# Performance work log

Hardware: AMD Instinct MI355X
Metric: run time of the kernel (lower is better)

The kernel has to match this reference:

```python
import jax, jax.numpy as jnp
import numpy as np

ALPHA = 0.2  # LeakyReLU negative slope
NEG_INF = -9e15


def setup_inputs() -> dict:
    key = jax.random.key(0)
    k1, k2, k3, k4 = jax.random.split(key, 4)
    N, IN_F, OUT_F = 8192, 512, 256
    h = jax.random.normal(k1, (N, IN_F), dtype=jnp.float32)
    adj = jax.random.randint(k2, (N, N), 0, 2).astype(jnp.float32)
    # xavier_uniform for torch Linear weights
    limW = float(np.sqrt(6.0 / (IN_F + OUT_F)))
    W = jax.random.uniform(k3, (OUT_F, IN_F), dtype=jnp.float32, minval=-limW, maxval=limW)
    lima = float(np.sqrt(6.0 / (2 * OUT_F + 1)))
    a_vec = jax.random.uniform(k4, (2 * OUT_F,), dtype=jnp.float32, minval=-lima, maxval=lima)
    return {"h": h, "adj": adj, "W": W, "a_vec": a_vec}


def reference(h, adj, W, a_vec):
    # Wh = W(h), torch Linear: h @ W.T  -> [N, out]
    Wh = h @ W.T
    F_out = W.shape[0]
    # e_ij = leakyrelu(a . [Wh_i, Wh_j]) = leakyrelu(a1.Wh_i + a2.Wh_j)
    s_src = Wh @ a_vec[:F_out]   # [N] contribution of row i
    s_dst = Wh @ a_vec[F_out:]   # [N] contribution of col j
    e = jax.nn.leaky_relu(s_src[:, None] + s_dst[None, :], negative_slope=ALPHA)  # [N, N]
    scores = jnp.where(adj > 0, e, jnp.float32(NEG_INF))
    attention = jax.nn.softmax(scores, axis=1)
    # dropout is identity in eval mode
    h_prime = attention @ Wh  # [N, out]
    return h_prime, attention
```

## Files before the change

### kernel.cpp

```cpp
#include <hip/hip_runtime.h>
#include <stdint.h>

#define N_NODES 8192
#define IN_F    512
#define OUT_F   256
#define ALPHA   0.2f

typedef __attribute__((ext_vector_type(8))) short bf16x8;
typedef __attribute__((ext_vector_type(4))) float f32x4;

__device__ __forceinline__ uint32_t f32_to_bf16(float f) {
    union { float f; uint32_t u; } v; v.f = f;
    uint32_t u = v.u;
    return (u + 0x7fffu + ((u >> 16) & 1u)) >> 16;
}

__global__ __launch_bounds__(256) void k0_wvec(
    const float* __restrict__ W, const float* __restrict__ a_vec,
    float* __restrict__ w12)
{
    const int t  = threadIdx.x;
    const int nb = blockIdx.x * 8;
    float a1lo = 0.f, a1hi = 0.f, a2lo = 0.f, a2hi = 0.f;
    #pragma unroll
    for (int q = 0; q < 8; q++) {
        int n = nb + q;
        float lo = W[(size_t)n * IN_F + t];
        float hi = W[(size_t)n * IN_F + t + 256];
        float a1 = a_vec[n], a2 = a_vec[OUT_F + n];
        a1lo = fmaf(lo, a1, a1lo); a1hi = fmaf(hi, a1, a1hi);
        a2lo = fmaf(lo, a2, a2lo); a2hi = fmaf(hi, a2, a2hi);
    }
    atomicAdd(&w12[t], a1lo);       atomicAdd(&w12[t + 256], a1hi);
    atomicAdd(&w12[512 + t], a2lo); atomicAdd(&w12[512 + t + 256], a2hi);
}

__global__ __launch_bounds__(256) void ks_svec(
    const float* __restrict__ h, const float* __restrict__ w12,
    float* __restrict__ s_src, float* __restrict__ s_dst)
{
    __shared__ float sw[1024];
    const int t = threadIdx.x;
    #pragma unroll
    for (int q = 0; q < 4; q++) sw[q * 256 + t] = w12[q * 256 + t];
    __syncthreads();
    const int w = t >> 6, ln = t & 63;
    const int i = blockIdx.x * 4 + w;
    const float* hr = h + (size_t)i * IN_F + ln * 8;
    float4 h0 = *(const float4*)hr;
    float4 h1 = *(const float4*)(hr + 4);
    const float* w1 = sw + ln * 8;
    const float* w2 = sw + 512 + ln * 8;
    float v1 = h0.x*w1[0] + h0.y*w1[1] + h0.z*w1[2] + h0.w*w1[3]
             + h1.x*w1[4] + h1.y*w1[5] + h1.z*w1[6] + h1.w*w1[7];
    float v2 = h0.x*w2[0] + h0.y*w2[1] + h0.z*w2[2] + h0.w*w2[3]
             + h1.x*w2[4] + h1.y*w2[5] + h1.z*w2[6] + h1.w*w2[7];
    #pragma unroll
    for (int off = 32; off >= 1; off >>= 1) {
        v1 += __shfl_xor(v1, off, 64);
        v2 += __shfl_xor(v2, off, 64);
    }
    if (ln == 0) { s_src[i] = v1; s_dst[i] = v2; }
}

__global__ __launch_bounds__(256) void k1_wh_pack(
    const float* __restrict__ h, const float* __restrict__ W,
    uint16_t* __restrict__ whf)
{
    const int n0 = blockIdx.x * 64, i0 = blockIdx.y * 64;
    const int t  = threadIdx.x;
    const int tn = t & 15, tm = t >> 4;

    __shared__ float As[32][68];
    __shared__ float Bs[32][68];

    float acc[4][4];
    #pragma unroll
    for (int i = 0; i < 4; i++)
        #pragma unroll
        for (int j = 0; j < 4; j++) acc[i][j] = 0.f;

    for (int k0 = 0; k0 < IN_F; k0 += 32) {
        __syncthreads();
        #pragma unroll
        for (int q = 0; q < 2; q++) {
            int u   = q * 256 + t;
            int row = u >> 3;
            int kf  = (u & 7) * 4;
            float4 va = *(const float4*)&h[(size_t)(i0 + row) * IN_F + k0 + kf];
            As[kf + 0][row] = va.x; As[kf + 1][row] = va.y;
            As[kf + 2][row] = va.z; As[kf + 3][row] = va.w;
            float4 vb = *(const float4*)&W[(size_t)(n0 + row) * IN_F + k0 + kf];
            Bs[kf + 0][row] = vb.x; Bs[kf + 1][row] = vb.y;
            Bs[kf + 2][row] = vb.z; Bs[kf + 3][row] = vb.w;
        }
        __syncthreads();
        #pragma unroll
        for (int kk = 0; kk < 32; kk++) {
            float a[4], b[4];
            *(float4*)a = *(const float4*)&As[kk][tm * 4];
            *(float4*)b = *(const float4*)&Bs[kk][tn * 4];
            #pragma unroll
            for (int i = 0; i < 4; i++)
                #pragma unroll
                for (int j = 0; j < 4; j++) acc[i][j] = fmaf(a[i], b[j], acc[i][j]);
        }
    }

    #pragma unroll
    for (int ii = 0; ii < 4; ii++) {
        int gr = i0 + tm * 4 + ii;
        int ck = gr >> 5;
        int lr = (gr >> 3) & 3;
        int jj = gr & 7;
        #pragma unroll
        for (int jn = 0; jn < 4; jn++) {
            int gc   = n0 + tn * 4 + jn;
            int c    = ck * 16 + (gc >> 4);
            int lane = (gc & 15) + lr * 16;
            whf[(size_t)c * 512 + lane * 8 + jj] = (uint16_t)f32_to_bf16(acc[ii][jn]);
        }
    }
}

__global__ __launch_bounds__(256) void k2_mask_l(
    const float* __restrict__ adj, const float* __restrict__ s_src,
    const float* __restrict__ s_dst, uint64_t* __restrict__ mask,
    float* __restrict__ l_out)
{
    const int i = blockIdx.x;
    const int t = threadIdx.x, w = t >> 6, ln = t & 63;
    const float si = s_src[i];
    const float4* rowv = (const float4*)(adj + (size_t)i * N_NODES);
    const float4* sdv  = (const float4*)s_dst;
    float acc = 0.f;
    #pragma unroll 2
    for (int it = 0; it < 8; it++) {
        int jb = it * 4 + w;
        int v4 = jb * 64 + ln;
        float4 a  = rowv[v4];
        float4 sd = sdv[v4];
        uint64_t b0 = __ballot(a.x > 0.f);
        uint64_t b1 = __ballot(a.y > 0.f);
        uint64_t b2 = __ballot(a.z > 0.f);
        uint64_t b3 = __ballot(a.w > 0.f);
        if (ln == 0) {
            uint64_t* mw = mask + (size_t)i * 128 + jb * 4;
            mw[0] = b0; mw[1] = b1; mw[2] = b2; mw[3] = b3;
        }
        float x, e;
        x = si + sd.x; e = fmaxf(x, ALPHA * x); if (a.x > 0.f) acc += __expf(e);
        x = si + sd.y; e = fmaxf(x, ALPHA * x); if (a.y > 0.f) acc += __expf(e);
        x = si + sd.z; e = fmaxf(x, ALPHA * x); if (a.z > 0.f) acc += __expf(e);
        x = si + sd.w; e = fmaxf(x, ALPHA * x); if (a.w > 0.f) acc += __expf(e);
    }
    #pragma unroll
    for (int off = 32; off >= 1; off >>= 1) acc += __shfl_xor(acc, off, 64);
    __shared__ float red[4];
    if (ln == 0) red[w] = acc;
    __syncthreads();
    if (t == 0) l_out[i] = (red[0] + red[1]) + (red[2] + red[3]);
}

__global__ __launch_bounds__(256, 4) void k3_att_gemm(
    const uint64_t* __restrict__ mask, const float* __restrict__ s_src,
    const float* __restrict__ s_dst, const float* __restrict__ l_in,
    const uint16_t* __restrict__ whf, float* __restrict__ att_out,
    float* __restrict__ partial)
{
    const int rb = blockIdx.x, jc = blockIdx.y;
    const int i0 = rb * 32, jbase = jc * 2048;
    const int t = threadIdx.x, w = t >> 6, ln = t & 63;
    const int mh = w & 1, kh = w >> 1;

    const int m   = mh * 16 + (ln & 15);
    const int kof = (ln >> 4) * 8;
    const int gi  = i0 + m;

    const float sim = s_src[gi];
    const float il  = 1.0f / l_in[gi];

    f32x4 acc[16];
    #pragma unroll
    for (int b = 0; b < 16; b++) acc[b] = (f32x4){0.f, 0.f, 0.f, 0.f};

    const uint64_t* mrow = mask + (size_t)gi * 128 + (jbase >> 8) * 4;
    uint64_t mwv[4];

    for (int it = 0; it < 32; it++) {
        const int j0 = jbase + it * 64;

        if ((it & 3) == 0) {
            const uint64_t* mp = mrow + (it >> 2) * 4;
            mwv[0] = mp[0]; mwv[1] = mp[1]; mwv[2] = mp[2]; mwv[3] = mp[3];
        }

        const float* sp = s_dst + j0 + kh * 32 + kof;
        float4 sd0 = *(const float4*)sp;
        float4 sd1 = *(const float4*)(sp + 4);
        float sdv[8] = {sd0.x, sd0.y, sd0.z, sd0.w, sd1.x, sd1.y, sd1.z, sd1.w};

        const int bbase = ((it & 3) << 4) + (kh << 3) + (kof >> 2);
        float p[8];
        #pragma unroll
        for (int jj = 0; jj < 8; jj++) {
            float x  = sim + sdv[jj];
            float e  = fmaxf(x, ALPHA * x);
            float pe = __expf(e) * il;
            int bidx = bbase + (jj >> 2);
            p[jj] = ((mwv[jj & 3] >> bidx) & 1ull) ? pe : 0.f;
        }

        float* go = att_out + (size_t)gi * N_NODES + j0 + kh * 32 + kof;
        __builtin_nontemporal_store(*(f32x4*)&p[0], (f32x4*)go);
        __builtin_nontemporal_store(*(f32x4*)&p[4], (f32x4*)(go + 4));

        union { bf16x8 v; uint32_t u[4]; } pk;
        #pragma unroll
        for (int q = 0; q < 4; q++)
            pk.u[q] = f32_to_bf16(p[2 * q]) | (f32_to_bf16(p[2 * q + 1]) << 16);
        bf16x8 af = pk.v;

        const uint16_t* src = whf + (((size_t)(j0 >> 5) + kh) << 13) + ln * 8;
        #pragma unroll
        for (int nl = 0; nl < 16; nl++) {
            bf16x8 bfr = *(const bf16x8*)(src + nl * 512);
            acc[nl] = __builtin_amdgcn_mfma_f32_16x16x32_bf16(af, bfr, acc[nl], 0, 0, 0);
        }
    }

    __shared__ float red[2][16][257];
    const int lr = (ln >> 4) * 4;
    if (kh == 1) {
        #pragma unroll
        for (int nl = 0; nl < 16; nl++)
            #pragma unroll
            for (int r = 0; r < 4; r++)
                red[mh][lr + r][nl * 16 + (ln & 15)] = acc[nl][r];
    }
    __syncthreads();
    if (kh == 0) {
        float* pbase = partial + (size_t)jc * ((size_t)N_NODES * OUT_F);
        const int gr0 = i0 + mh * 16 + lr;
        #pragma unroll
        for (int nl = 0; nl < 16; nl++) {
            int gc = nl * 16 + (ln & 15);
            #pragma unroll
            for (int r = 0; r < 4; r++)
                pbase[(size_t)(gr0 + r) * OUT_F + gc] = acc[nl][r] + red[mh][lr + r][gc];
        }
    }
}

__global__ __launch_bounds__(256) void k4_reduce(
    const float* __restrict__ partial, float* __restrict__ hp)
{
    const size_t S = (size_t)N_NODES * OUT_F;
    int idx = (blockIdx.x * 256 + threadIdx.x) * 4;
    float4 a = *(const float4*)(partial + idx);
    float4 b = *(const float4*)(partial + S + idx);
    float4 c = *(const float4*)(partial + 2 * S + idx);
    float4 d = *(const float4*)(partial + 3 * S + idx);
    float4 o;
    o.x = (a.x + b.x) + (c.x + d.x);
    o.y = (a.y + b.y) + (c.y + d.y);
    o.z = (a.z + b.z) + (c.z + d.z);
    o.w = (a.w + b.w) + (c.w + d.w);
    *(float4*)(hp + idx) = o;
}

extern "C" void kernel_launch(void* const* d_in, const int* in_sizes, int n_in,
                              void* d_out, int out_size, void* d_ws, size_t ws_size,
                              hipStream_t stream) {
    (void)in_sizes; (void)n_in; (void)out_size; (void)ws_size;
    const float* h     = (const float*)d_in[0];
    const float* adj   = (const float*)d_in[1];
    const float* W     = (const float*)d_in[2];
    const float* a_vec = (const float*)d_in[3];

    char* ws = (char*)d_ws;
    uint16_t* whf  = (uint16_t*)(ws);
    uint64_t* mask = (uint64_t*)(ws + ((size_t)4 << 20));
    float* partial = (float*)(ws + ((size_t)12 << 20));
    float* w12     = (float*)(ws + ((size_t)44 << 20));
    float* s_src   = (float*)(ws + ((size_t)44 << 20) + 16384);
    float* s_dst   = (float*)(ws + ((size_t)44 << 20) + 16384 + 32768);
    float* l_buf   = (float*)(ws + ((size_t)44 << 20) + 16384 + 65536);

    float* hp  = (float*)d_out;
    float* att = hp + (size_t)N_NODES * OUT_F;

    hipMemsetAsync(w12, 0, 4096, stream);
    k0_wvec<<<32, 256, 0, stream>>>(W, a_vec, w12);
    ks_svec<<<2048, 256, 0, stream>>>(h, w12, s_src, s_dst);
    k1_wh_pack<<<dim3(4, 128), 256, 0, stream>>>(h, W, whf);
    k2_mask_l<<<8192, 256, 0, stream>>>(adj, s_src, s_dst, mask, l_buf);
    k3_att_gemm<<<dim3(256, 4), 256, 0, stream>>>(mask, s_src, s_dst, l_buf, whf, att, partial);
    k4_reduce<<<2048, 256, 0, stream>>>(partial, hp);
}
```

Before: 727.4 us.

## Double-buffer Wh B-tiles into LDS via async global-to-LDS copies

The attention GEMM kernel now stages each 64-row slice of bf16 Wh into a double-buffered LDS tile with global_load_lds, prefetching the next slice while MFMAs consume the current one, rather than having each wave load B fragments straight from global memory. The 64KB buffer is reused for the final reduction scratch, and launch bounds drop to 2 blocks per SU to fit the LDS. The aim is to share B loads across the two M-half waves and hide global latency. The cost is a block-wide barrier and full vmcnt drain every iteration, plus lower occupancy. The mask/row-sum kernel loop is also fully unrolled.

New measurement: 682.5 us. 6.2% less time.

```diff
diff --git a/kernel.cpp b/kernel.cpp
--- a/kernel.cpp
+++ b/kernel.cpp
@@ -13,6 +13,12 @@
     union { float f; uint32_t u; } v; v.f = f;
     uint32_t u = v.u;
     return (u + 0x7fffu + ((u >> 16) & 1u)) >> 16;
+}
+
+__device__ __forceinline__ void async_copy16(const void* g, void* l) {
+    __builtin_amdgcn_global_load_lds(
+        (const __attribute__((address_space(1))) uint32_t*)g,
+        (__attribute__((address_space(3))) uint32_t*)l, 16, 0, 0);
 }
 
 __global__ __launch_bounds__(256) void k0_wvec(
@@ -134,7 +140,7 @@
     const float4* rowv = (const float4*)(adj + (size_t)i * N_NODES);
     const float4* sdv  = (const float4*)s_dst;
     float acc = 0.f;
-    #pragma unroll 2
+    #pragma unroll
     for (int it = 0; it < 8; it++) {
         int jb = it * 4 + w;
         int v4 = jb * 64 + ln;
@@ -162,7 +168,7 @@
     if (t == 0) l_out[i] = (red[0] + red[1]) + (red[2] + red[3]);
 }
 
-__global__ __launch_bounds__(256, 4) void k3_att_gemm(
+__global__ __launch_bounds__(256, 2) void k3_att_gemm(
     const uint64_t* __restrict__ mask, const float* __restrict__ s_src,
     const float* __restrict__ s_dst, const float* __restrict__ l_in,
     const uint16_t* __restrict__ whf, float* __restrict__ att_out,
@@ -173,6 +179,8 @@
     const int t = threadIdx.x, w = t >> 6, ln = t & 63;
     const int mh = w & 1, kh = w >> 1;
 
+    __shared__ uint16_t whf_lds[2][16384];
+
     const int m   = mh * 16 + (ln & 15);
     const int kof = (ln >> 4) * 8;
     const int gi  = i0 + m;
@@ -187,8 +195,30 @@
     const uint64_t* mrow = mask + (size_t)gi * 128 + (jbase >> 8) * 4;
     uint64_t mwv[4];
 
+    {
+        const uint16_t* src = whf + ((size_t)(jbase >> 5)) * 8192;
+        #pragma unroll
+        for (int q = 0; q < 8; q++) {
+            int c = w * 8 + q;
+            async_copy16(src + (size_t)c * 512 + ln * 8, &whf_lds[0][c * 512]);
+        }
+        asm volatile("s_waitcnt vmcnt(0)" ::: "memory");
+        __builtin_amdgcn_s_barrier();
+    }
+
     for (int it = 0; it < 32; it++) {
-        const int j0 = jbase + it * 64;
+        const int j0  = jbase + it * 64;
+        const int cur = it & 1;
+
+        if (it < 31) {
+            const uint16_t* src = whf + ((size_t)((j0 + 64) >> 5)) * 8192;
+            #pragma unroll
+            for (int q = 0; q < 8; q++) {
+                int c = w * 8 + q;
+                async_copy16(src + (size_t)c * 512 + ln * 8,
+                             &whf_lds[cur ^ 1][c * 512]);
+            }
+        }
 
         if ((it & 3) == 0) {
             const uint64_t* mp = mrow + (it >> 2) * 4;
@@ -221,15 +251,19 @@
             pk.u[q] = f32_to_bf16(p[2 * q]) | (f32_to_bf16(p[2 * q + 1]) << 16);
         bf16x8 af = pk.v;
 
-        const uint16_t* src = whf + (((size_t)(j0 >> 5) + kh) << 13) + ln * 8;
+        const uint16_t* bl = &whf_lds[cur][kh * 8192 + ln * 8];
         #pragma unroll
         for (int nl = 0; nl < 16; nl++) {
-            bf16x8 bfr = *(const bf16x8*)(src + nl * 512);
+            bf16x8 bfr = *(const bf16x8*)(bl + nl * 512);
             acc[nl] = __builtin_amdgcn_mfma_f32_16x16x32_bf16(af, bfr, acc[nl], 0, 0, 0);
         }
-    }
-
-    __shared__ float red[2][16][257];
+
+        asm volatile("s_waitcnt vmcnt(0)" ::: "memory");
+        __builtin_amdgcn_s_barrier();
+    }
+
+    __syncthreads();
+    float (*red)[16][257] = (float (*)[16][257])whf_lds;
     const int lr = (ln >> 4) * 4;
     if (kh == 1) {
         #pragma unroll
```

## Stage Wh tiles in LDS with double-buffered async copies, split GEMM by output columns

Applied to the files above, without the earlier changes.

The attention+GEMM kernel now stages the bf16 Wh tiles into double-buffered LDS using global_load_lds async copies, prefetching the next K-slice while the current one is consumed. The mask bits and s_dst values are also staged in LDS. Waves now split the 256 output columns in halves instead of splitting K, so the LDS cross-wave reduction goes away. Only one half of the waves writes the attention matrix, and occupancy is lowered to 3 blocks per SM to make room for the LDS. The goal is to hide global-load latency for Wh and cut redundant global reads, at the cost of twice as many iterations with a barrier each and duplicated exp computation across wave halves.

Result: no change. 727.0 us (-0.1%).

```diff
diff --git a/kernel.cpp b/kernel.cpp
--- a/kernel.cpp
+++ b/kernel.cpp
@@ -13,6 +13,12 @@
     union { float f; uint32_t u; } v; v.f = f;
     uint32_t u = v.u;
     return (u + 0x7fffu + ((u >> 16) & 1u)) >> 16;
+}
+
+__device__ __forceinline__ void async_copy16(const void* g, void* l) {
+    __builtin_amdgcn_global_load_lds(
+        (const __attribute__((address_space(1))) uint32_t*)g,
+        (__attribute__((address_space(3))) uint32_t*)l, 16, 0, 0);
 }
 
 __global__ __launch_bounds__(256) void k0_wvec(
@@ -134,7 +140,7 @@
     const float4* rowv = (const float4*)(adj + (size_t)i * N_NODES);
     const float4* sdv  = (const float4*)s_dst;
     float acc = 0.f;
-    #pragma unroll 2
+    #pragma unroll
     for (int it = 0; it < 8; it++) {
         int jb = it * 4 + w;
         int v4 = jb * 64 + ln;
@@ -162,7 +168,7 @@
     if (t == 0) l_out[i] = (red[0] + red[1]) + (red[2] + red[3]);
 }
 
-__global__ __launch_bounds__(256, 4) void k3_att_gemm(
+__global__ __launch_bounds__(256, 3) void k3_att_gemm(
     const uint64_t* __restrict__ mask, const float* __restrict__ s_src,
     const float* __restrict__ s_dst, const float* __restrict__ l_in,
     const uint16_t* __restrict__ whf, float* __restrict__ att_out,
@@ -171,7 +177,30 @@
     const int rb = blockIdx.x, jc = blockIdx.y;
     const int i0 = rb * 32, jbase = jc * 2048;
     const int t = threadIdx.x, w = t >> 6, ln = t & 63;
-    const int mh = w & 1, kh = w >> 1;
+    const int mh = w & 1, nh = w >> 1;
+
+    __shared__ uint16_t whf_lds[2][8192];
+    __shared__ float    sdt[2048];
+    __shared__ uint64_t mtab[32 * 33];
+
+    {
+        const float4* s4 = (const float4*)(s_dst + jbase);
+        ((float4*)sdt)[t * 2]     = s4[t * 2];
+        ((float4*)sdt)[t * 2 + 1] = s4[t * 2 + 1];
+        int r = t >> 3, c = (t & 7) * 4;
+        const uint64_t* mr = mask + (size_t)(i0 + r) * 128 + (jbase >> 8) * 4 + c;
+        uint64_t m0 = mr[0], m1 = mr[1], m2 = mr[2], m3 = mr[3];
+        uint64_t* md = &mtab[r * 33 + c];
+        md[0] = m0; md[1] = m1; md[2] = m2; md[3] = m3;
+        const uint16_t* src = whf + ((size_t)(jbase >> 5)) * 8192;
+        #pragma unroll
+        for (int q = 0; q < 4; q++) {
+            int cchunk = w * 4 + q;
+            async_copy16(src + (size_t)cchunk * 512 + ln * 8,
+                         &whf_lds[0][cchunk * 512]);
+        }
+        __builtin_amdgcn_sched_barrier(0);
+    }
 
     const int m   = mh * 16 + (ln & 15);
     const int kof = (ln >> 4) * 8;
@@ -180,27 +209,40 @@
     const float sim = s_src[gi];
     const float il  = 1.0f / l_in[gi];
 
-    f32x4 acc[16];
-    #pragma unroll
-    for (int b = 0; b < 16; b++) acc[b] = (f32x4){0.f, 0.f, 0.f, 0.f};
-
-    const uint64_t* mrow = mask + (size_t)gi * 128 + (jbase >> 8) * 4;
+    f32x4 acc[8];
+    #pragma unroll
+    for (int b = 0; b < 8; b++) acc[b] = (f32x4){0.f, 0.f, 0.f, 0.f};
+
+    __syncthreads();
+
     uint64_t mwv[4];
 
-    for (int it = 0; it < 32; it++) {
-        const int j0 = jbase + it * 64;
-
-        if ((it & 3) == 0) {
-            const uint64_t* mp = mrow + (it >> 2) * 4;
+    for (int it = 0; it < 64; it++) {
+        const int cur = it & 1;
+
+        if (it < 63) {
+            const uint16_t* src =
+                whf + ((size_t)(jbase >> 5) + it + 1) * 8192;
+            #pragma unroll
+            for (int q = 0; q < 4; q++) {
+                int cchunk = w * 4 + q;
+                async_copy16(src + (size_t)cchunk * 512 + ln * 8,
+                             &whf_lds[cur ^ 1][cchunk * 512]);
+            }
+        }
+        __builtin_amdgcn_sched_barrier(0);
+
+        if ((it & 7) == 0) {
+            const uint64_t* mp = &mtab[m * 33 + (it >> 3) * 4];
             mwv[0] = mp[0]; mwv[1] = mp[1]; mwv[2] = mp[2]; mwv[3] = mp[3];
         }
 
-        const float* sp = s_dst + j0 + kh * 32 + kof;
+        const float* sp = sdt + it * 32 + kof;
         float4 sd0 = *(const float4*)sp;
         float4 sd1 = *(const float4*)(sp + 4);
         float sdv[8] = {sd0.x, sd0.y, sd0.z, sd0.w, sd1.x, sd1.y, sd1.z, sd1.w};
 
-        const int bbase = ((it & 3) << 4) + (kh << 3) + (kof >> 2);
+        const int bbase = ((it & 7) << 3) + (kof >> 2);
         float p[8];
         #pragma unroll
         for (int jj = 0; jj < 8; jj++) {
@@ -211,44 +253,38 @@
             p[jj] = ((mwv[jj & 3] >> bidx) & 1ull) ? pe : 0.f;
         }
 
-        float* go = att_out + (size_t)gi * N_NODES + j0 + kh * 32 + kof;
-        __builtin_nontemporal_store(*(f32x4*)&p[0], (f32x4*)go);
-        __builtin_nontemporal_store(*(f32x4*)&p[4], (f32x4*)(go + 4));
-
         union { bf16x8 v; uint32_t u[4]; } pk;
         #pragma unroll
         for (int q = 0; q < 4; q++)
             pk.u[q] = f32_to_bf16(p[2 * q]) | (f32_to_bf16(p[2 * q + 1]) << 16);
         bf16x8 af = pk.v;
 
-        const uint16_t* src = whf + (((size_t)(j0 >> 5) + kh) << 13) + ln * 8;
-        #pragma unroll
-        for (int nl = 0; nl < 16; nl++) {
-            bf16x8 bfr = *(const bf16x8*)(src + nl * 512);
+        const uint16_t* bl = &whf_lds[cur][nh * 8 * 512 + ln * 8];
+        #pragma unroll
+        for (int nl = 0; nl < 8; nl++) {
+            bf16x8 bfr = *(const bf16x8*)(bl + nl * 512);
             acc[nl] = __builtin_amdgcn_mfma_f32_16x16x32_bf16(af, bfr, acc[nl], 0, 0, 0);
         }
-    }
-
-    __shared__ float red[2][16][257];
-    const int lr = (ln >> 4) * 4;
-    if (kh == 1) {
-        #pragma unroll
-        for (int nl = 0; nl < 16; nl++)
-            #pragma unroll
-            for (int r = 0; r < 4; r++)
-                red[mh][lr + r][nl * 16 + (ln & 15)] = acc[nl][r];
-    }
-    __syncthreads();
-    if (kh == 0) {
-        float* pbase = partial + (size_t)jc * ((size_t)N_NODES * OUT_F);
-        const int gr0 = i0 + mh * 16 + lr;
-        #pragma unroll
-        for (int nl = 0; nl < 16; nl++) {
-            int gc = nl * 16 + (ln & 15);
-            #pragma unroll
-            for (int r = 0; r < 4; r++)
-                pbase[(size_t)(gr0 + r) * OUT_F + gc] = acc[nl][r] + red[mh][lr + r][gc];
-        }
+
+        if (nh == 0) {
+            float* go = att_out + (size_t)gi * N_NODES + jbase + it * 32 + kof;
+            __builtin_nontemporal_store(*(f32x4*)&p[0], (f32x4*)go);
+            __builtin_nontemporal_store(*(f32x4*)&p[4], (f32x4*)(go + 4));
+        }
+
+        if (nh == 0) asm volatile("s_waitcnt vmcnt(2)" ::: "memory");
+        else         asm volatile("s_waitcnt vmcnt(0)" ::: "memory");
+        __builtin_amdgcn_s_barrier();
+    }
+
+    float* pbase = partial + (size_t)jc * ((size_t)N_NODES * OUT_F);
+    const int gr0 = i0 + mh * 16 + (ln >> 4) * 4;
+    #pragma unroll
+    for (int nl = 0; nl < 8; nl++) {
+        int gc = nh * 128 + nl * 16 + (ln & 15);
+        #pragma unroll
+        for (int r = 0; r < 4; r++)
+            pbase[(size_t)(gr0 + r) * OUT_F + gc] = acc[nl][r];
     }
 }
 
```
